# Kernel optimization log

Measured on AMD Instinct MI355X. Metric: run time of the kernel, lower is better.

## Reference

```python
import jax, jax.numpy as jnp
import numpy as np

N = 8192
IN_F = 128
OUT_F = 128
ALPHA = 0.2  # LeakyReLU negative slope
NEG_INF = -9e15


def setup_inputs() -> dict:
    key = jax.random.key(0)
    k1, k2, k3, k4 = jax.random.split(key, 4)
    h = jax.random.normal(k1, (N, IN_F), dtype=jnp.float32)
    adj = jax.random.randint(k2, (N, N), 0, 2, dtype=jnp.int32)
    # nn.Linear(in, out, bias=False).weight is (out, in); store as (in, out) for h @ W
    W = jax.random.normal(k3, (IN_F, OUT_F), dtype=jnp.float32) * (1.0 / np.sqrt(IN_F))
    # a: (2*out_features, 1), xavier_uniform with gain=1.414
    limit = 1.414 * np.sqrt(6.0 / (2 * OUT_F + 1))
    a = jax.random.uniform(k4, (2 * OUT_F, 1), dtype=jnp.float32, minval=-limit, maxval=limit)
    return {"h": h, "adj": adj, "W": W, "a": a}


def reference(h, adj, W, a):
    Wh = h @ W  # (N, OUT_F)
    a1 = a[:OUT_F, 0]   # score contribution from source node i
    a2 = a[OUT_F:, 0]   # score contribution from target node j
    # e_ij = leakyrelu(Wh_i . a1 + Wh_j . a2) -- avoids the O(N^2 * 2F) concat
    s1 = Wh @ a1  # (N,)
    s2 = Wh @ a2  # (N,)
    e = jax.nn.leaky_relu(s1[:, None] + s2[None, :], negative_slope=ALPHA)  # (N, N)
    masked = jnp.where(adj > 0, e, NEG_INF)
    attention = jax.nn.softmax(masked, axis=1)  # (N, N)
    # dropout is a no-op in eval mode
    h_prime = attention @ Wh  # (N, OUT_F)
    return jax.nn.elu(h_prime)  # concat=True -> ELU
```

## Files before the change

### kernel.cpp

```cpp
#include <hip/hip_runtime.h>
#include <cstdint>
#include <cstddef>


#define NROW 8192
#define FDIM 128

typedef _Float16 f16;
typedef f16 f16x8 __attribute__((ext_vector_type(8)));
typedef float f32x4 __attribute__((ext_vector_type(4)));
typedef float f32x16 __attribute__((ext_vector_type(16)));

#define WS_WHT 0u
#define WS_BP  (2u*1024u*1024u)
#define WS_S12 (4u*1024u*1024u)
#define WS_RC  (WS_S12 + 64u*1024u)
#define WS_EF  (WS_RC + 128u*1024u)
#define WS_M2  (WS_EF + 64u*1024u)
#define WS_PWS (WS_M2 + 4u*1024u)

__global__ __launch_bounds__(256) void kA_wh_pack(const float* __restrict__ h,
                                                  const float* __restrict__ W,
                                                  const int* __restrict__ adj,
                                                  f16* __restrict__ WhT,
                                                  f16* __restrict__ Bp,
                                                  unsigned* __restrict__ bm,
                                                  unsigned* __restrict__ M2key) {
  __shared__ float hT[128 * 36];
  const int bid = (int)blockIdx.x;
  const int t = (int)threadIdx.x;

  if (bid >= 256) {
    const int pb = bid - 256;
    const int w = t >> 6, l = t & 63;
    const int r = pb * 4 + w;
    const int rg = r >> 5, m = r & 31;
    const int* ap = adj + (size_t)r * NROW + l;
    unsigned* bp = bm + (size_t)rg * (256 * 32) + m;
    for (int jb = 0; jb < NROW; jb += 256) {
      int v0 = ap[jb];
      int v1 = ap[jb + 64];
      int v2 = ap[jb + 128];
      int v3 = ap[jb + 192];
      unsigned long long m0 = __ballot(v0 > 0);
      unsigned long long m1 = __ballot(v1 > 0);
      unsigned long long m2 = __ballot(v2 > 0);
      unsigned long long m3 = __ballot(v3 > 0);
      if (l == 0) {
        int jw = jb >> 5;
        bp[(size_t)(jw + 0) * 32] = (unsigned)m0;
        bp[(size_t)(jw + 1) * 32] = (unsigned)(m0 >> 32);
        bp[(size_t)(jw + 2) * 32] = (unsigned)m1;
        bp[(size_t)(jw + 3) * 32] = (unsigned)(m1 >> 32);
        bp[(size_t)(jw + 4) * 32] = (unsigned)m2;
        bp[(size_t)(jw + 5) * 32] = (unsigned)(m2 >> 32);
        bp[(size_t)(jw + 6) * 32] = (unsigned)m3;
        bp[(size_t)(jw + 7) * 32] = (unsigned)(m3 >> 32);
      }
    }
    return;
  }

  const int rb = bid * 32;
  if (bid == 0 && t == 0) *M2key = 0u;
  const f32x4* hv = (const f32x4*)(h + (size_t)rb * FDIM);
#pragma unroll
  for (int i = 0; i < 4; ++i) {
    int fidx = t + i * 256;
    f32x4 v = hv[fidx];
    int e0 = fidx * 4;
    int r = e0 >> 7, k = e0 & 127;
    hT[(k + 0) * 36 + r] = v[0];
    hT[(k + 1) * 36 + r] = v[1];
    hT[(k + 2) * 36 + r] = v[2];
    hT[(k + 3) * 36 + r] = v[3];
  }
  __syncthreads();
  const int f = t & 127, rh = t >> 7;
  f32x4 z = {0.f, 0.f, 0.f, 0.f};
  f32x4 acc0 = z, acc1 = z, acc2 = z, acc3 = z;
  for (int k = 0; k < 128; ++k) {
    float w = W[k * FDIM + f];
    const f32x4* hp = (const f32x4*)(hT + k * 36 + rh * 16);
    acc0 += hp[0] * w;
    acc1 += hp[1] * w;
    acc2 += hp[2] * w;
    acc3 += hp[3] * w;
  }
  union { f16 hx[16]; uint4 u[2]; } pk;
#pragma unroll
  for (int q = 0; q < 4; ++q) {
    pk.hx[0 + q]  = (f16)acc0[q];
    pk.hx[4 + q]  = (f16)acc1[q];
    pk.hx[8 + q]  = (f16)acc2[q];
    pk.hx[12 + q] = (f16)acc3[q];
  }
  uint4* dst = (uint4*)(WhT + (size_t)f * NROW + rb + rh * 16);
  dst[0] = pk.u[0];
  dst[1] = pk.u[1];
  f16* bdst = Bp + ((size_t)((bid * 2 + rh) * 4 + (f >> 5)) * 64 + (f & 31)) * 8;
  *(uint4*)bdst = pk.u[0];
  *(uint4*)(bdst + 256) = pk.u[1];
}

__global__ __launch_bounds__(256) void k1b_s(const f16* __restrict__ WhT,
                                             const float* __restrict__ a,
                                             float2* __restrict__ s12,
                                             unsigned* __restrict__ M2key) {
  __shared__ float part[2][4][64];
  const int l = (int)threadIdx.x & 63;
  const int fc = (int)threadIdx.x >> 6;
  const int r = (int)blockIdx.x * 64 + l;
  float s1 = 0.f, s2 = 0.f;
  for (int f = fc * 32; f < fc * 32 + 32; ++f) {
    float w = (float)WhT[(size_t)f * NROW + r];
    s1 = fmaf(w, a[f], s1);
    s2 = fmaf(w, a[128 + f], s2);
  }
  part[0][fc][l] = s1;
  part[1][fc][l] = s2;
  __syncthreads();
  if (fc == 0) {
    s1 = part[0][0][l] + part[0][1][l] + part[0][2][l] + part[0][3][l];
    s2 = part[1][0][l] + part[1][1][l] + part[1][2][l] + part[1][3][l];
    s12[r] = make_float2(s1, s2);
    float mx = s2;
#pragma unroll
    for (int off = 32; off; off >>= 1) mx = fmaxf(mx, __shfl_xor(mx, off, 64));
    if (l == 0) {
      unsigned key = __float_as_uint(mx);
      key = (key & 0x80000000u) ? ~key : (key | 0x80000000u);
      atomicMax(M2key, key);
    }
  }
}

__global__ __launch_bounds__(256) void k1c_prep(const float2* __restrict__ s12,
                                                const unsigned* __restrict__ M2key,
                                                float4* __restrict__ RC,
                                                float2* __restrict__ EF) {
  int j = (int)blockIdx.x * 256 + (int)threadIdx.x;
  unsigned key = *M2key;
  float M2 = (key & 0x80000000u) ? __uint_as_float(key ^ 0x80000000u)
                                 : __uint_as_float(~key);
  float2 s = s12[j];
  float c = s.x + M2;
  c = fmaxf(c, 0.2f * c);
  RC[j] = make_float4(__expf(-s.x), __expf(s.x - c), __expf(0.2f * s.x - c), 0.f);
  EF[j] = make_float2(__expf(s.y), __expf(0.2f * s.y));
}

__global__ __launch_bounds__(256) void k2_main(const unsigned* __restrict__ bm,
                                               const f16* __restrict__ Bp,
                                               const float4* __restrict__ RC,
                                               const float* __restrict__ EF,
                                               float* __restrict__ Pws,
                                               float* __restrict__ Dws,
                                               int jspan) {
  const int tid = (int)threadIdx.x;
  const int L = tid & 63, w = tid >> 6;
  const int wid = (int)blockIdx.x * 4 + w;
  const int rg = wid & 255;
  const int c = wid >> 8;
  const int rb = rg * 32;
  const int m = L & 31, kb = L >> 5;
  const int row = rb + m;
  const int j0 = c * jspan;
  const int niter = jspan >> 5;

  const float4 rc = RC[row];
  const float tau = rc.x, kap1 = rc.y, kap2 = rc.z;

  const unsigned* wbase = bm + ((size_t)rg * 256 + (size_t)(j0 >> 5)) * 32 + m;
  const f32x4* ep = (const f32x4*)(EF + 2 * (j0 + kb * 8));
  const f16* bp = Bp + (size_t)(j0 >> 4) * 2048 + L * 8;

  unsigned WD  = wbase[0];
  unsigned WDn = wbase[32];
  f32x4 E0 = ep[0], E1 = ep[1], E2 = ep[2], E3 = ep[3];
  f32x4 E4 = ep[8], E5 = ep[9], E6 = ep[10], E7 = ep[11];

  f32x16 zz = {0.f};
  f32x16 acc[4] = {zz, zz, zz, zz};
  float dloc = 0.f;

  for (int it = 0; it < niter; ++it) {
    const f16* bt = bp + (size_t)it * 4096;
    f16x8 B00 = *(const f16x8*)(bt);
    f16x8 B01 = *(const f16x8*)(bt + 512);
    f16x8 B02 = *(const f16x8*)(bt + 1024);
    f16x8 B03 = *(const f16x8*)(bt + 1536);
    f16x8 B10 = *(const f16x8*)(bt + 2048);
    f16x8 B11 = *(const f16x8*)(bt + 2560);
    f16x8 B12 = *(const f16x8*)(bt + 3072);
    f16x8 B13 = *(const f16x8*)(bt + 3584);

    const unsigned u0 = WD >> (kb * 8);
    const unsigned u1 = u0 >> 16;
    f16x8 af0, af1;
    {
      float p;
      p = (E0[0] > tau) ? E0[0] * kap1 : E0[1] * kap2; p = (u0 & 1u)   ? p : 0.f; dloc += p; af0[0] = (f16)p;
      p = (E0[2] > tau) ? E0[2] * kap1 : E0[3] * kap2; p = (u0 & 2u)   ? p : 0.f; dloc += p; af0[1] = (f16)p;
      p = (E1[0] > tau) ? E1[0] * kap1 : E1[1] * kap2; p = (u0 & 4u)   ? p : 0.f; dloc += p; af0[2] = (f16)p;
      p = (E1[2] > tau) ? E1[2] * kap1 : E1[3] * kap2; p = (u0 & 8u)   ? p : 0.f; dloc += p; af0[3] = (f16)p;
      p = (E2[0] > tau) ? E2[0] * kap1 : E2[1] * kap2; p = (u0 & 16u)  ? p : 0.f; dloc += p; af0[4] = (f16)p;
      p = (E2[2] > tau) ? E2[2] * kap1 : E2[3] * kap2; p = (u0 & 32u)  ? p : 0.f; dloc += p; af0[5] = (f16)p;
      p = (E3[0] > tau) ? E3[0] * kap1 : E3[1] * kap2; p = (u0 & 64u)  ? p : 0.f; dloc += p; af0[6] = (f16)p;
      p = (E3[2] > tau) ? E3[2] * kap1 : E3[3] * kap2; p = (u0 & 128u) ? p : 0.f; dloc += p; af0[7] = (f16)p;
      p = (E4[0] > tau) ? E4[0] * kap1 : E4[1] * kap2; p = (u1 & 1u)   ? p : 0.f; dloc += p; af1[0] = (f16)p;
      p = (E4[2] > tau) ? E4[2] * kap1 : E4[3] * kap2; p = (u1 & 2u)   ? p : 0.f; dloc += p; af1[1] = (f16)p;
      p = (E5[0] > tau) ? E5[0] * kap1 : E5[1] * kap2; p = (u1 & 4u)   ? p : 0.f; dloc += p; af1[2] = (f16)p;
      p = (E5[2] > tau) ? E5[2] * kap1 : E5[3] * kap2; p = (u1 & 8u)   ? p : 0.f; dloc += p; af1[3] = (f16)p;
      p = (E6[0] > tau) ? E6[0] * kap1 : E6[1] * kap2; p = (u1 & 16u)  ? p : 0.f; dloc += p; af1[4] = (f16)p;
      p = (E6[2] > tau) ? E6[2] * kap1 : E6[3] * kap2; p = (u1 & 32u)  ? p : 0.f; dloc += p; af1[5] = (f16)p;
      p = (E7[0] > tau) ? E7[0] * kap1 : E7[1] * kap2; p = (u1 & 64u)  ? p : 0.f; dloc += p; af1[6] = (f16)p;
      p = (E7[2] > tau) ? E7[2] * kap1 : E7[3] * kap2; p = (u1 & 128u) ? p : 0.f; dloc += p; af1[7] = (f16)p;
    }

    int nx = (it + 2 < niter) ? (it + 2) : (niter - 1);
    WD = WDn;
    WDn = wbase[(size_t)nx * 32];
    int adv = (it < niter - 1) ? 1 : 0;
    ep += adv * 16;
    E0 = ep[0]; E1 = ep[1]; E2 = ep[2]; E3 = ep[3];
    E4 = ep[8]; E5 = ep[9]; E6 = ep[10]; E7 = ep[11];

    __builtin_amdgcn_s_setprio(1);
    acc[0] = __builtin_amdgcn_mfma_f32_32x32x16_f16(af0, B00, acc[0], 0, 0, 0);
    acc[1] = __builtin_amdgcn_mfma_f32_32x32x16_f16(af0, B01, acc[1], 0, 0, 0);
    acc[2] = __builtin_amdgcn_mfma_f32_32x32x16_f16(af0, B02, acc[2], 0, 0, 0);
    acc[3] = __builtin_amdgcn_mfma_f32_32x32x16_f16(af0, B03, acc[3], 0, 0, 0);
    acc[0] = __builtin_amdgcn_mfma_f32_32x32x16_f16(af1, B10, acc[0], 0, 0, 0);
    acc[1] = __builtin_amdgcn_mfma_f32_32x32x16_f16(af1, B11, acc[1], 0, 0, 0);
    acc[2] = __builtin_amdgcn_mfma_f32_32x32x16_f16(af1, B12, acc[2], 0, 0, 0);
    acc[3] = __builtin_amdgcn_mfma_f32_32x32x16_f16(af1, B13, acc[3], 0, 0, 0);
    __builtin_amdgcn_s_setprio(0);
  }

  dloc += __shfl_xor(dloc, 32, 64);
  if (L < 32) Dws[(size_t)c * NROW + row] = dloc;

  float* P = Pws + ((size_t)c * NROW + rb) * FDIM + (L & 31);
#pragma unroll
  for (int nt = 0; nt < 4; ++nt) {
#pragma unroll
    for (int reg = 0; reg < 16; ++reg) {
      int rr = (reg & 3) + 8 * (reg >> 2) + 4 * kb;
      P[(size_t)rr * FDIM + nt * 32] = acc[nt][reg];
    }
  }
}

__global__ __launch_bounds__(256) void k3_comb(const float* __restrict__ Pws,
                                               const float* __restrict__ Dws,
                                               float* __restrict__ out, int S) {
  int g = (int)blockIdx.x * 256 + (int)threadIdx.x;
  int r = g >> 5, f4 = g & 31;
  f32x4 s = {0.f, 0.f, 0.f, 0.f};
  float den = 0.f;
  for (int c2 = 0; c2 < S; ++c2) {
    s += *(const f32x4*)(Pws + ((size_t)c2 * NROW + r) * FDIM + f4 * 4);
    den += Dws[(size_t)c2 * NROW + r];
  }
  float inv = 1.0f / den;
  f32x4 o;
#pragma unroll
  for (int e = 0; e < 4; ++e) {
    float x = s[e] * inv;
    o[e] = x > 0.f ? x : expm1f(x);
  }
  *(f32x4*)(out + (size_t)r * FDIM + f4 * 4) = o;
}

extern "C" void kernel_launch(void* const* d_in, const int* in_sizes, int n_in,
                              void* d_out, int out_size, void* d_ws, size_t ws_size,
                              hipStream_t stream) {
  const float* h = (const float*)d_in[0];
  const int* adj = (const int*)d_in[1];
  const float* W = (const float*)d_in[2];
  const float* a = (const float*)d_in[3];
  float* out = (float*)d_out;
  char* ws = (char*)d_ws;
  f16* WhT = (f16*)(ws + WS_WHT);
  f16* Bp = (f16*)(ws + WS_BP);
  float2* s12 = (float2*)(ws + WS_S12);
  float4* RC = (float4*)(ws + WS_RC);
  float2* EF = (float2*)(ws + WS_EF);
  unsigned* M2 = (unsigned*)(ws + WS_M2);

  const size_t partial_bytes = (size_t)NROW * FDIM * 4;
  const size_t bm_bytes = (size_t)8 * 1024 * 1024;
  int S = (ws_size >= WS_PWS + 8 * partial_bytes + 8 * (size_t)NROW * 4 + bm_bytes) ? 8 : 2;
  float* Pws = (float*)(ws + WS_PWS);
  float* Dws = (float*)(ws + WS_PWS + (size_t)S * partial_bytes);
  unsigned* BM = (unsigned*)(ws + WS_PWS + (size_t)S * partial_bytes + (size_t)S * NROW * 4);
  int jspan = NROW / S;

  kA_wh_pack<<<dim3(2304), dim3(256), 0, stream>>>(h, W, adj, WhT, Bp, BM, M2);
  k1b_s<<<dim3(128), dim3(256), 0, stream>>>(WhT, a, s12, M2);
  k1c_prep<<<dim3(32), dim3(256), 0, stream>>>(s12, M2, RC, EF);
  k2_main<<<dim3(64 * S), dim3(256), 0, stream>>>(BM, Bp, RC, (const float*)EF, Pws, Dws, jspan);
  k3_comb<<<dim3(1024), dim3(256), 0, stream>>>(Pws, Dws, out, S);
}
```

Baseline: 430.1 us.

## Fuse score computation into Wh kernel, vectorize adjacency bitpacking, drop atomic max

Computes s1/s2 inside the Wh projection kernel from fp32 accumulators staged in shared memory, which removes the WhT fp16 buffer and the separate k1b_s launch. The global max of s2 becomes per-block partial maxima that k1c_prep reduces itself, replacing the atomicMax on an encoded key. Adjacency bitpacking now reads int4 per lane and builds 32-bit words with shuffles instead of four scalar loads and ballots per iteration. This saves one launch, one global round trip of Wh and the atomics, at the cost of extra shared memory and syncs in kA. Scores now come from fp32 rather than fp16-rounded Wh, so the numbers shift slightly.

Measured after the change: 431.0 us. About the same (+0.2%).

```diff
diff --git a/kernel.cpp b/kernel.cpp
--- a/kernel.cpp
+++ b/kernel.cpp
@@ -11,7 +11,6 @@
 typedef float f32x4 __attribute__((ext_vector_type(4)));
 typedef float f32x16 __attribute__((ext_vector_type(16)));
 
-#define WS_WHT 0u
 #define WS_BP  (2u*1024u*1024u)
 #define WS_S12 (4u*1024u*1024u)
 #define WS_RC  (WS_S12 + 64u*1024u)
@@ -21,12 +20,13 @@
 
 __global__ __launch_bounds__(256) void kA_wh_pack(const float* __restrict__ h,
                                                   const float* __restrict__ W,
+                                                  const float* __restrict__ a,
                                                   const int* __restrict__ adj,
-                                                  f16* __restrict__ WhT,
                                                   f16* __restrict__ Bp,
                                                   unsigned* __restrict__ bm,
-                                                  unsigned* __restrict__ M2key) {
-  __shared__ float hT[128 * 36];
+                                                  float2* __restrict__ s12,
+                                                  float* __restrict__ M2v) {
+  __shared__ float smem[4736];
   const int bid = (int)blockIdx.x;
   const int t = (int)threadIdx.x;
 
@@ -35,34 +35,23 @@
     const int w = t >> 6, l = t & 63;
     const int r = pb * 4 + w;
     const int rg = r >> 5, m = r & 31;
-    const int* ap = adj + (size_t)r * NROW + l;
+    const int* ap = adj + (size_t)r * NROW;
     unsigned* bp = bm + (size_t)rg * (256 * 32) + m;
+    const int g = l >> 3;
     for (int jb = 0; jb < NROW; jb += 256) {
-      int v0 = ap[jb];
-      int v1 = ap[jb + 64];
-      int v2 = ap[jb + 128];
-      int v3 = ap[jb + 192];
-      unsigned long long m0 = __ballot(v0 > 0);
-      unsigned long long m1 = __ballot(v1 > 0);
-      unsigned long long m2 = __ballot(v2 > 0);
-      unsigned long long m3 = __ballot(v3 > 0);
-      if (l == 0) {
-        int jw = jb >> 5;
-        bp[(size_t)(jw + 0) * 32] = (unsigned)m0;
-        bp[(size_t)(jw + 1) * 32] = (unsigned)(m0 >> 32);
-        bp[(size_t)(jw + 2) * 32] = (unsigned)m1;
-        bp[(size_t)(jw + 3) * 32] = (unsigned)(m1 >> 32);
-        bp[(size_t)(jw + 4) * 32] = (unsigned)m2;
-        bp[(size_t)(jw + 5) * 32] = (unsigned)(m2 >> 32);
-        bp[(size_t)(jw + 6) * 32] = (unsigned)m3;
-        bp[(size_t)(jw + 7) * 32] = (unsigned)(m3 >> 32);
-      }
+      int4 v = *(const int4*)(ap + jb + 4 * l);
+      unsigned nib = (v.x > 0 ? 1u : 0u) | (v.y > 0 ? 2u : 0u) |
+                     (v.z > 0 ? 4u : 0u) | (v.w > 0 ? 8u : 0u);
+      unsigned word = nib << (4 * (l & 7));
+      word |= (unsigned)__shfl_xor((int)word, 1, 64);
+      word |= (unsigned)__shfl_xor((int)word, 2, 64);
+      word |= (unsigned)__shfl_xor((int)word, 4, 64);
+      if ((l & 7) == 0) bp[(size_t)((jb >> 5) + g) * 32] = word;
     }
     return;
   }
 
   const int rb = bid * 32;
-  if (bid == 0 && t == 0) *M2key = 0u;
   const f32x4* hv = (const f32x4*)(h + (size_t)rb * FDIM);
 #pragma unroll
   for (int i = 0; i < 4; ++i) {
@@ -70,10 +59,10 @@
     f32x4 v = hv[fidx];
     int e0 = fidx * 4;
     int r = e0 >> 7, k = e0 & 127;
-    hT[(k + 0) * 36 + r] = v[0];
-    hT[(k + 1) * 36 + r] = v[1];
-    hT[(k + 2) * 36 + r] = v[2];
-    hT[(k + 3) * 36 + r] = v[3];
+    smem[(k + 0) * 36 + r] = v[0];
+    smem[(k + 1) * 36 + r] = v[1];
+    smem[(k + 2) * 36 + r] = v[2];
+    smem[(k + 3) * 36 + r] = v[3];
   }
   __syncthreads();
   const int f = t & 127, rh = t >> 7;
@@ -81,7 +70,7 @@
   f32x4 acc0 = z, acc1 = z, acc2 = z, acc3 = z;
   for (int k = 0; k < 128; ++k) {
     float w = W[k * FDIM + f];
-    const f32x4* hp = (const f32x4*)(hT + k * 36 + rh * 16);
+    const f32x4* hp = (const f32x4*)(smem + k * 36 + rh * 16);
     acc0 += hp[0] * w;
     acc1 += hp[1] * w;
     acc2 += hp[2] * w;
@@ -95,54 +84,64 @@
     pk.hx[8 + q]  = (f16)acc2[q];
     pk.hx[12 + q] = (f16)acc3[q];
   }
-  uint4* dst = (uint4*)(WhT + (size_t)f * NROW + rb + rh * 16);
-  dst[0] = pk.u[0];
-  dst[1] = pk.u[1];
   f16* bdst = Bp + ((size_t)((bid * 2 + rh) * 4 + (f >> 5)) * 64 + (f & 31)) * 8;
   *(uint4*)bdst = pk.u[0];
   *(uint4*)(bdst + 256) = pk.u[1];
-}
-
-__global__ __launch_bounds__(256) void k1b_s(const f16* __restrict__ WhT,
-                                             const float* __restrict__ a,
-                                             float2* __restrict__ s12,
-                                             unsigned* __restrict__ M2key) {
-  __shared__ float part[2][4][64];
-  const int l = (int)threadIdx.x & 63;
-  const int fc = (int)threadIdx.x >> 6;
-  const int r = (int)blockIdx.x * 64 + l;
-  float s1 = 0.f, s2 = 0.f;
-  for (int f = fc * 32; f < fc * 32 + 32; ++f) {
-    float w = (float)WhT[(size_t)f * NROW + r];
-    s1 = fmaf(w, a[f], s1);
-    s2 = fmaf(w, a[128 + f], s2);
-  }
-  part[0][fc][l] = s1;
-  part[1][fc][l] = s2;
+
   __syncthreads();
-  if (fc == 0) {
-    s1 = part[0][0][l] + part[0][1][l] + part[0][2][l] + part[0][3][l];
-    s2 = part[1][0][l] + part[1][1][l] + part[1][2][l] + part[1][3][l];
-    s12[r] = make_float2(s1, s2);
-    float mx = s2;
-#pragma unroll
-    for (int off = 32; off; off >>= 1) mx = fmaxf(mx, __shfl_xor(mx, off, 64));
-    if (l == 0) {
-      unsigned key = __float_as_uint(mx);
-      key = (key & 0x80000000u) ? ~key : (key | 0x80000000u);
-      atomicMax(M2key, key);
+#pragma unroll
+  for (int q = 0; q < 4; ++q) {
+    smem[(rh * 16 + 0  + q) * 132 + f] = acc0[q];
+    smem[(rh * 16 + 4  + q) * 132 + f] = acc1[q];
+    smem[(rh * 16 + 8  + q) * 132 + f] = acc2[q];
+    smem[(rh * 16 + 12 + q) * 132 + f] = acc3[q];
+  }
+  __syncthreads();
+  {
+    const int row = t & 31, fc = t >> 5;
+    const float* wrow = smem + row * 132 + fc * 16;
+    float s1 = 0.f, s2 = 0.f;
+#pragma unroll
+    for (int ff = 0; ff < 16; ++ff) {
+      float wv = wrow[ff];
+      int fg = fc * 16 + ff;
+      s1 = fmaf(wv, a[fg], s1);
+      s2 = fmaf(wv, a[128 + fg], s2);
+    }
+    float* part = smem + 4224;
+    __syncthreads();
+    part[0 * 256 + fc * 32 + row] = s1;
+    part[1 * 256 + fc * 32 + row] = s2;
+    __syncthreads();
+    if (t < 32) {
+      float s1t = 0.f, s2t = 0.f;
+#pragma unroll
+      for (int c2 = 0; c2 < 8; ++c2) {
+        s1t += part[c2 * 32 + t];
+        s2t += part[256 + c2 * 32 + t];
+      }
+      s12[rb + t] = make_float2(s1t, s2t);
+      float mx = s2t;
+#pragma unroll
+      for (int off = 16; off; off >>= 1) mx = fmaxf(mx, __shfl_xor(mx, off, 64));
+      if (t == 0) M2v[bid] = mx;
     }
   }
 }
 
 __global__ __launch_bounds__(256) void k1c_prep(const float2* __restrict__ s12,
-                                                const unsigned* __restrict__ M2key,
+                                                const float* __restrict__ M2v,
                                                 float4* __restrict__ RC,
                                                 float2* __restrict__ EF) {
-  int j = (int)blockIdx.x * 256 + (int)threadIdx.x;
-  unsigned key = *M2key;
-  float M2 = (key & 0x80000000u) ? __uint_as_float(key ^ 0x80000000u)
-                                 : __uint_as_float(~key);
+  __shared__ float red[4];
+  const int t = (int)threadIdx.x;
+  float v = M2v[t];
+#pragma unroll
+  for (int off = 32; off; off >>= 1) v = fmaxf(v, __shfl_xor(v, off, 64));
+  if ((t & 63) == 0) red[t >> 6] = v;
+  __syncthreads();
+  float M2 = fmaxf(fmaxf(red[0], red[1]), fmaxf(red[2], red[3]));
+  int j = (int)blockIdx.x * 256 + t;
   float2 s = s12[j];
   float c = s.x + M2;
   c = fmaxf(c, 0.2f * c);
@@ -282,12 +281,11 @@
   const float* a = (const float*)d_in[3];
   float* out = (float*)d_out;
   char* ws = (char*)d_ws;
-  f16* WhT = (f16*)(ws + WS_WHT);
   f16* Bp = (f16*)(ws + WS_BP);
   float2* s12 = (float2*)(ws + WS_S12);
   float4* RC = (float4*)(ws + WS_RC);
   float2* EF = (float2*)(ws + WS_EF);
-  unsigned* M2 = (unsigned*)(ws + WS_M2);
+  float* M2v = (float*)(ws + WS_M2);
 
   const size_t partial_bytes = (size_t)NROW * FDIM * 4;
   const size_t bm_bytes = (size_t)8 * 1024 * 1024;
@@ -297,9 +295,8 @@
   unsigned* BM = (unsigned*)(ws + WS_PWS + (size_t)S * partial_bytes + (size_t)S * NROW * 4);
   int jspan = NROW / S;
 
-  kA_wh_pack<<<dim3(2304), dim3(256), 0, stream>>>(h, W, adj, WhT, Bp, BM, M2);
-  k1b_s<<<dim3(128), dim3(256), 0, stream>>>(WhT, a, s12, M2);
-  k1c_prep<<<dim3(32), dim3(256), 0, stream>>>(s12, M2, RC, EF);
+  kA_wh_pack<<<dim3(2304), dim3(256), 0, stream>>>(h, W, a, adj, Bp, BM, s12, M2v);
+  k1c_prep<<<dim3(32), dim3(256), 0, stream>>>(s12, M2v, RC, EF);
   k2_main<<<dim3(64 * S), dim3(256), 0, stream>>>(BM, Bp, RC, (const float*)EF, Pws, Dws, jspan);
   k3_comb<<<dim3(1024), dim3(256), 0, stream>>>(Pws, Dws, out, S);
 }
```
